# Kernel tuning notes

Hardware: AMD Instinct MI355X
Metric: run time of the kernel (lower is better)

## Reference

```python
import jax, jax.numpy as jnp
import numpy as np

B, T_Q, T_K, H = 16, 1024, 1024, 1024


def _linear_params(key, fan_in, fan_out):
    kw, kb = jax.random.split(key)
    bound = 1.0 / np.sqrt(fan_in)
    W = jax.random.uniform(kw, (fan_out, fan_in), jnp.float32, -bound, bound)
    b = jax.random.uniform(kb, (fan_out,), jnp.float32, -bound, bound)
    return W, b


def setup_inputs() -> dict:
    key = jax.random.key(0)
    ks = jax.random.split(key, 6)
    query = jax.random.normal(ks[0], (B, T_Q, H), jnp.float32)
    keys = jax.random.normal(ks[1], (B, T_K, H), jnp.float32)
    values = jax.random.normal(ks[2], (B, T_K, H), jnp.float32)
    Wq, bq = _linear_params(ks[3], H, H)
    Wk, bk = _linear_params(ks[4], H, H)
    Wo, bo = _linear_params(ks[5], H, H)
    return {"query": query, "keys": keys, "values": values,
            "Wq": Wq, "bq": bq, "Wk": Wk, "bk": bk, "Wo": Wo, "bo": bo}


def reference(query, keys, values, Wq, bq, Wk, bk, Wo, bo):
    # Linear projections (torch Linear: x @ W.T + b)
    q = jnp.einsum('bth,oh->bto', query, Wq) + bq   # (B, T_Q, H)
    k = jnp.einsum('bsh,oh->bso', keys, Wk) + bk    # (B, T_K, H)
    # Unscaled scores -> softmax over key axis (dropout is identity at eval)
    scores = jnp.einsum('bto,bso->bts', q, k)       # (B, T_Q, T_K)
    attn = jax.nn.softmax(scores, axis=-1)
    ctx = jnp.einsum('bts,bsh->bth', attn, values)  # note: raw values, value_fc unused in source
    ctx = ctx / jnp.sqrt(jnp.float32(values.shape[1]))
    out = jnp.einsum('bth,oh->bto', ctx, Wo) + bo
    return out
```

## Files before the change

kernel.cpp:

```cpp
#include <hip/hip_runtime.h>
#include <math.h>

typedef __attribute__((ext_vector_type(4))) float f32x4;
typedef __attribute__((ext_vector_type(8))) _Float16 h16x8;
typedef __attribute__((ext_vector_type(8))) short s16x8;
typedef __attribute__((ext_vector_type(4))) short s16x4;

__device__ inline unsigned short f2h(float f) {
    union { _Float16 h; unsigned short u; } v; v.h = (_Float16)f; return v.u;
}
__device__ inline float h2f(unsigned short u) {
    union { unsigned short u; _Float16 h; } v; v.u = u; return (float)v.h;
}

__device__ inline void async16(const void* g, void* l) {
    __builtin_amdgcn_global_load_lds(
        (const __attribute__((address_space(1))) unsigned int*)g,
        (__attribute__((address_space(3))) unsigned int*)l, 16, 0, 0);
}

__device__ inline void xcd_swizzle(int& bx, int& by, int& bz) {
    const long gx = gridDim.x, gy = gridDim.y;
    const long nwg = gx * gy * (long)gridDim.z;
    const long hw  = ((long)blockIdx.z * gy + blockIdx.y) * gx + blockIdx.x;
    const long qq = nwg >> 3, rr = nwg & 7;
    const long xcd = hw & 7, pos = hw >> 3;
    const long lg = (xcd < rr) ? xcd * (qq + 1) + pos
                               : rr * (qq + 1) + (xcd - rr) * qq + pos;
    bx = (int)(lg % gx);
    const long rem = lg / gx;
    by = (int)(rem % gy);
    bz = (int)(rem / gy);
}

#define BM2 128
#define BN2 256
#define BK2 32

__device__ inline h16x8 ld_frag32(const char* smem, unsigned base, int row, int kbyte) {
    unsigned off = base + (unsigned)(row * 64) + (unsigned)(kbyte ^ ((row & 3) << 4));
    return *(const h16x8*)(smem + off);
}

template<int OM>
__global__ __launch_bounds__(512, 4)
void gemm128(const unsigned short* __restrict__ A,
             const unsigned short* __restrict__ B,
             const float* __restrict__ bias,
             void* __restrict__ C, int N, int lenK, int pitch,
             long sA, long sB, long sC, long sBias, float scale)
{
    __shared__ __align__(16) char smem[49152];

    const int tid  = threadIdx.x;
    const int wv   = tid >> 6;
    const int lane = tid & 63;
    const int wr = wv >> 2, wc = wv & 3;
    const int lrow = lane & 15;
    const int kq16 = (lane >> 4) * 16;

    int bx, by, bz; xcd_swizzle(bx, by, bz);
    const int n0 = bx * BN2;
    const int m0 = by * BM2;

    const unsigned short* Ag = A + (long)bz * sA;
    const unsigned short* Bg = B + (long)bz * sB;
    const int NT = lenK / BK2;

    auto stage = [&](int t) {
        const unsigned db = (unsigned)((t & 1) * 24576);
        {
            int r = tid >> 2, s = tid & 3, ss = s ^ (r & 3);
            async16((const char*)Ag + ((long)(m0 + r) * pitch + t * BK2 + ss * 8) * 2,
                    smem + db + (unsigned)(wv << 10));
        }
#pragma unroll
        for (int l = 0; l < 2; ++l) {
            int idx = l * 512 + tid;
            int r = idx >> 2, s = idx & 3, ss = s ^ (r & 3);
            async16((const char*)Bg + ((long)(n0 + r) * pitch + t * BK2 + ss * 8) * 2,
                    smem + db + 8192u + (unsigned)(l * 8192) + (unsigned)(wv << 10));
        }
    };

    f32x4 acc[4][4];
#pragma unroll
    for (int i = 0; i < 4; ++i)
#pragma unroll
        for (int j = 0; j < 4; ++j) acc[i][j] = (f32x4){0.f, 0.f, 0.f, 0.f};

    const unsigned Abase = (unsigned)(wr * 4096);
    const unsigned Bbase = 8192u + (unsigned)(wc * 4096);

    stage(0);
    __syncthreads();

#pragma unroll 2
    for (int t = 0; t < NT; ++t) {
        const unsigned db = (unsigned)((t & 1) * 24576);
        if (t + 1 < NT) stage(t + 1);
        h16x8 afr[4], bfr[4];
#pragma unroll
        for (int f = 0; f < 4; ++f) {
            afr[f] = ld_frag32(smem, db + Abase, f * 16 + lrow, kq16);
            bfr[f] = ld_frag32(smem, db + Bbase, f * 16 + lrow, kq16);
        }
#pragma unroll
        for (int mi = 0; mi < 4; ++mi)
#pragma unroll
            for (int j = 0; j < 4; ++j)
                acc[mi][j] = __builtin_amdgcn_mfma_f32_16x16x32_f16(
                    afr[mi], bfr[j], acc[mi][j], 0, 0, 0);
        __syncthreads();
    }

#pragma unroll
    for (int j = 0; j < 4; ++j) {
        const int col = n0 + wc * 64 + j * 16 + lrow;
        const float bb = bias ? bias[(long)bz * sBias + col] : 0.f;
#pragma unroll
        for (int mi = 0; mi < 4; ++mi) {
#pragma unroll
            for (int r = 0; r < 4; ++r) {
                const long row = m0 + wr * 64 + mi * 16 + (lane >> 4) * 4 + r;
                const float v = acc[mi][j][r] * scale + bb;
                const long idx = (long)bz * sC + row * (long)N + col;
                if constexpr (OM == 0) ((float*)C)[idx] = v;
                else                   ((unsigned short*)C)[idx] = f2h(v);
            }
        }
    }
}


__global__ __launch_bounds__(256)
void conv2_f16(const float* __restrict__ a, const float* __restrict__ b,
               unsigned short* __restrict__ oa, unsigned short* __restrict__ ob, long n)
{
    const long stride = (long)gridDim.x * 256 * 16;
    const long t0 = ((long)blockIdx.x * 256 + threadIdx.x) * 16;
    for (long i = t0; i < n; i += stride) {
        float4 v0 = *(const float4*)(a + i);
        float4 v1 = *(const float4*)(a + i + 4);
        float4 v2 = *(const float4*)(a + i + 8);
        float4 v3 = *(const float4*)(a + i + 12);
        s16x8 o0 = {(short)f2h(v0.x), (short)f2h(v0.y), (short)f2h(v0.z), (short)f2h(v0.w),
                    (short)f2h(v1.x), (short)f2h(v1.y), (short)f2h(v1.z), (short)f2h(v1.w)};
        s16x8 o1 = {(short)f2h(v2.x), (short)f2h(v2.y), (short)f2h(v2.z), (short)f2h(v2.w),
                    (short)f2h(v3.x), (short)f2h(v3.y), (short)f2h(v3.z), (short)f2h(v3.w)};
        *(s16x8*)(oa + i)     = o0;
        *(s16x8*)(oa + i + 8) = o1;
    }
    for (long i = t0; i < n; i += stride) {
        float4 v0 = *(const float4*)(b + i);
        float4 v1 = *(const float4*)(b + i + 4);
        float4 v2 = *(const float4*)(b + i + 8);
        float4 v3 = *(const float4*)(b + i + 12);
        s16x8 o0 = {(short)f2h(v0.x), (short)f2h(v0.y), (short)f2h(v0.z), (short)f2h(v0.w),
                    (short)f2h(v1.x), (short)f2h(v1.y), (short)f2h(v1.z), (short)f2h(v1.w)};
        s16x8 o1 = {(short)f2h(v2.x), (short)f2h(v2.y), (short)f2h(v2.z), (short)f2h(v2.w),
                    (short)f2h(v3.x), (short)f2h(v3.y), (short)f2h(v3.z), (short)f2h(v3.w)};
        *(s16x8*)(ob + i)     = o0;
        *(s16x8*)(ob + i + 8) = o1;
    }
}

__global__ __launch_bounds__(256)
void conv_f16(const float* __restrict__ in, unsigned short* __restrict__ out, int n)
{
    int i = (blockIdx.x * 256 + threadIdx.x) * 4;
    if (i >= n) return;
    float4 v = *(const float4*)(in + i);
    s16x4 o = {(short)f2h(v.x), (short)f2h(v.y), (short)f2h(v.z), (short)f2h(v.w)};
    *(s16x4*)(out + i) = o;
}

__global__ __launch_bounds__(256)
void transpose_vals(const float* __restrict__ in, unsigned short* __restrict__ out)
{
    __shared__ float tile[32][33];
    const int h0 = blockIdx.x * 32, t0 = blockIdx.y * 32;
    for (int z = blockIdx.z; z < 16; z += gridDim.z) {
        const long base = (long)z * 1024 * 1024;
        __syncthreads();
        for (int i = threadIdx.y; i < 32; i += 8)
            tile[i][threadIdx.x] = in[base + (long)(t0 + i) * 1024 + h0 + threadIdx.x];
        __syncthreads();
        for (int i = threadIdx.y; i < 32; i += 8)
            out[base + (long)(h0 + i) * 1024 + t0 + threadIdx.x] = f2h(tile[threadIdx.x][i]);
    }
}

__global__ __launch_bounds__(256)
void transpose2_f16(const float* __restrict__ inA, const float* __restrict__ inB,
                    unsigned short* __restrict__ outA, unsigned short* __restrict__ outB)
{
    __shared__ float tile[32][33];
    const float* in = blockIdx.z ? inB : inA;
    unsigned short* out = blockIdx.z ? outB : outA;
    const int h0 = blockIdx.x * 32, t0 = blockIdx.y * 32;
    for (int i = threadIdx.y; i < 32; i += 8)
        tile[i][threadIdx.x] = in[(long)(t0 + i) * 1024 + h0 + threadIdx.x];
    __syncthreads();
    for (int i = threadIdx.y; i < 32; i += 8)
        out[(long)(h0 + i) * 1024 + t0 + threadIdx.x] = f2h(tile[threadIdx.x][i]);
}

__global__ __launch_bounds__(256)
void w2_kernel(const float* __restrict__ Wk, const float* __restrict__ bq,
               float* __restrict__ w2)
{
    __shared__ float part[4][64];
    const int tx = threadIdx.x & 63;
    const int ty = threadIdx.x >> 6;
    const int h  = blockIdx.x * 64 + tx;
    float s = 0.f;
    for (int o = ty * 256; o < ty * 256 + 256; ++o)
        s = fmaf(Wk[(long)o * 1024 + h], bq[o], s);
    part[ty][tx] = s;
    __syncthreads();
    if (ty == 0) w2[h] = part[0][tx] + part[1][tx] + part[2][tx] + part[3][tx];
}

__global__ __launch_bounds__(256)
void matvec_v(const unsigned short* __restrict__ Xk, const float* __restrict__ w2,
              float* __restrict__ v)
{
    const int wave = threadIdx.x >> 6, lane = threadIdx.x & 63;
    const long row = (long)blockIdx.x * 4 + wave;
    const unsigned short* p = Xk + row * 1024 + lane * 16;
    float s = 0.f;
#pragma unroll
    for (int c = 0; c < 2; ++c) {
        s16x8 hv = *(const s16x8*)(p + c * 8);
#pragma unroll
        for (int e = 0; e < 8; ++e)
            s = fmaf(h2f((unsigned short)hv[e]), w2[lane * 16 + c * 8 + e], s);
    }
#pragma unroll
    for (int off = 1; off < 64; off <<= 1) s += __shfl_xor(s, off);
    if (lane == 0) v[row] = s;
}

__global__ __launch_bounds__(256)
void reduce4(const float* __restrict__ p, unsigned short* __restrict__ MT)
{
    const long i = ((long)blockIdx.x * 256 + threadIdx.x) * 4;
    const long S = 1024L * 1024;
    float4 a = *(const float4*)(p + i);
    float4 b = *(const float4*)(p + S + i);
    float4 c = *(const float4*)(p + 2 * S + i);
    float4 d = *(const float4*)(p + 3 * S + i);
    s16x4 o = {(short)f2h(a.x + b.x + c.x + d.x), (short)f2h(a.y + b.y + c.y + d.y),
               (short)f2h(a.z + b.z + c.z + d.z), (short)f2h(a.w + b.w + c.w + d.w)};
    *(s16x4*)(MT + i) = o;
}

__global__ __launch_bounds__(256)
void softmax_wave(unsigned short* __restrict__ S)
{
    const int wave = threadIdx.x >> 6, lane = threadIdx.x & 63;
    for (long row = (long)blockIdx.x * 4 + wave; row < 16384; row += (long)gridDim.x * 4) {
        unsigned short* p = S + row * 1024;
        s16x8 ra = *(s16x8*)(p + lane * 8);
        s16x8 rb = *(s16x8*)(p + 512 + lane * 8);
        float va[8], vb[8];
        float m = -3.0e38f;
#pragma unroll
        for (int e = 0; e < 8; ++e) {
            va[e] = h2f((unsigned short)ra[e]); m = fmaxf(m, va[e]);
            vb[e] = h2f((unsigned short)rb[e]); m = fmaxf(m, vb[e]);
        }
#pragma unroll
        for (int off = 1; off < 64; off <<= 1) m = fmaxf(m, __shfl_xor(m, off));
        float s = 0.f;
#pragma unroll
        for (int e = 0; e < 8; ++e) {
            va[e] = expf(va[e] - m); s += va[e];
            vb[e] = expf(vb[e] - m); s += vb[e];
        }
#pragma unroll
        for (int off = 1; off < 64; off <<= 1) s += __shfl_xor(s, off);
        const float inv = 1.f / s;
        s16x8 oa, ob;
#pragma unroll
        for (int e = 0; e < 8; ++e) {
            oa[e] = (short)f2h(va[e] * inv);
            ob[e] = (short)f2h(vb[e] * inv);
        }
        *(s16x8*)(p + lane * 8)       = oa;
        *(s16x8*)(p + 512 + lane * 8) = ob;
    }
}

extern "C" void kernel_launch(void* const* d_in, const int* in_sizes, int n_in,
                              void* d_out, int out_size, void* d_ws, size_t ws_size,
                              hipStream_t stream)
{
    const float* query  = (const float*)d_in[0];
    const float* keys   = (const float*)d_in[1];
    const float* values = (const float*)d_in[2];
    const float* Wq     = (const float*)d_in[3];
    const float* bq     = (const float*)d_in[4];
    const float* Wk     = (const float*)d_in[5];
    const float* bk     = (const float*)d_in[6];
    const float* Wo     = (const float*)d_in[7];
    const float* bo     = (const float*)d_in[8];
    (void)bk;

    const int  T = 1024, H = 1024;
    const long NE = 16384L * 1024;
    const long NW = 1024L * 1024;

    size_t need = (size_t)(NE * 4 + NW * 12 + 40960) * sizeof(unsigned short);
    if (ws_size < need) return;

    unsigned short* ws   = (unsigned short*)d_ws;
    unsigned short* Xq   = ws;
    unsigned short* Xk   = Xq + NE;
    unsigned short* vT   = Xk + NE;
    unsigned short* P1   = vT + NE;
    unsigned short* WqT  = P1 + NE;
    unsigned short* WkT  = WqT + NW;
    unsigned short* Woh  = WkT + NW;
    unsigned short* MT   = Woh + NW;
    float*          part = (float*)(MT + NW);
    float*          w2   = (float*)(MT + NW * 9);
    float*          vvec = w2 + 1024;
    unsigned short* sc   = Xq;
    unsigned short* ctx  = P1;

    conv2_f16<<<2048, 256, 0, stream>>>(query, keys, Xq, Xk, NE);
    transpose2_f16<<<dim3(32, 32, 2), dim3(32, 8), 0, stream>>>(Wq, Wk, WqT, WkT);
    conv_f16<<<1024, 256, 0, stream>>>(Wo, Woh, (int)NW);
    transpose_vals<<<dim3(32, 32, 4), dim3(32, 8), 0, stream>>>(values, vT);
    w2_kernel<<<16, 256, 0, stream>>>(Wk, bq, w2);

    gemm128<0><<<dim3(4, 8, 4), 512, 0, stream>>>(
        WkT, WqT, nullptr, part, 1024, 256, 1024, 256, 256, (long)NW, 0, 1.f);
    reduce4<<<1024, 256, 0, stream>>>(part, MT);

    gemm128<1><<<dim3(4, 128, 1), 512, 0, stream>>>(
        Xq, MT, nullptr, P1, H, H, H, 0, 0, 0, 0, 1.f);

    matvec_v<<<4096, 256, 0, stream>>>(Xk, w2, vvec);

    gemm128<1><<<dim3(4, 8, 16), 512, 0, stream>>>(
        P1, Xk, vvec, sc, T, H, H,
        (long)T * H, (long)T * H, (long)T * T, (long)T, 1.f);

    softmax_wave<<<2048, 256, 0, stream>>>(sc);

    gemm128<1><<<dim3(4, 8, 16), 512, 0, stream>>>(
        sc, vT, nullptr, ctx, H, T, T,
        (long)T * T, (long)T * H, (long)T * H, 0, 1.f / 32.f);

    gemm128<0><<<dim3(4, 128, 1), 512, 0, stream>>>(
        ctx, Woh, bo, d_out, H, H, H, 0, 0, 0, 0, 1.f);
}
```

Baseline: 294.0 us.

## Fuse query fp32-to-fp16 conversion into the first projection GEMM's A-tile load

Adds a GEMM variant that reads the fp32 query directly, converting to fp16 in registers before writing to shared memory, while B is still staged asynchronously. This drops the separate conversion pass over the 16M-element query tensor and its fp16 round trip through global memory. The A path now uses synchronous register loads instead of async LDS loads, so the GEMM reads twice as many bytes for A and may overlap loads less well.

```diff
diff --git a/kernel.cpp b/kernel.cpp
--- a/kernel.cpp
+++ b/kernel.cpp
@@ -132,37 +132,122 @@
     }
 }
 
-
-__global__ __launch_bounds__(256)
-void conv2_f16(const float* __restrict__ a, const float* __restrict__ b,
-               unsigned short* __restrict__ oa, unsigned short* __restrict__ ob, long n)
-{
-    const long stride = (long)gridDim.x * 256 * 16;
-    const long t0 = ((long)blockIdx.x * 256 + threadIdx.x) * 16;
-    for (long i = t0; i < n; i += stride) {
-        float4 v0 = *(const float4*)(a + i);
-        float4 v1 = *(const float4*)(a + i + 4);
-        float4 v2 = *(const float4*)(a + i + 8);
-        float4 v3 = *(const float4*)(a + i + 12);
-        s16x8 o0 = {(short)f2h(v0.x), (short)f2h(v0.y), (short)f2h(v0.z), (short)f2h(v0.w),
-                    (short)f2h(v1.x), (short)f2h(v1.y), (short)f2h(v1.z), (short)f2h(v1.w)};
-        s16x8 o1 = {(short)f2h(v2.x), (short)f2h(v2.y), (short)f2h(v2.z), (short)f2h(v2.w),
-                    (short)f2h(v3.x), (short)f2h(v3.y), (short)f2h(v3.z), (short)f2h(v3.w)};
-        *(s16x8*)(oa + i)     = o0;
-        *(s16x8*)(oa + i + 8) = o1;
-    }
-    for (long i = t0; i < n; i += stride) {
-        float4 v0 = *(const float4*)(b + i);
-        float4 v1 = *(const float4*)(b + i + 4);
-        float4 v2 = *(const float4*)(b + i + 8);
-        float4 v3 = *(const float4*)(b + i + 12);
-        s16x8 o0 = {(short)f2h(v0.x), (short)f2h(v0.y), (short)f2h(v0.z), (short)f2h(v0.w),
-                    (short)f2h(v1.x), (short)f2h(v1.y), (short)f2h(v1.z), (short)f2h(v1.w)};
-        s16x8 o1 = {(short)f2h(v2.x), (short)f2h(v2.y), (short)f2h(v2.z), (short)f2h(v2.w),
-                    (short)f2h(v3.x), (short)f2h(v3.y), (short)f2h(v3.z), (short)f2h(v3.w)};
-        *(s16x8*)(ob + i)     = o0;
-        *(s16x8*)(ob + i + 8) = o1;
-    }
+__global__ __launch_bounds__(512, 4)
+void gemm128_af32(const float* __restrict__ A,
+                  const unsigned short* __restrict__ B,
+                  const float* __restrict__ bias,
+                  unsigned short* __restrict__ C, int N, int lenK, int pitch,
+                  float scale)
+{
+    __shared__ __align__(16) char smem[49152];
+
+    const int tid  = threadIdx.x;
+    const int wv   = tid >> 6;
+    const int lane = tid & 63;
+    const int wr = wv >> 2, wc = wv & 3;
+    const int lrow = lane & 15;
+    const int kq16 = (lane >> 4) * 16;
+
+    int bx, by, bz; xcd_swizzle(bx, by, bz);
+    const int n0 = bx * BN2;
+    const int m0 = by * BM2;
+
+    const int NT = lenK / BK2;
+
+    const int ar = tid >> 2;
+    const int ac = tid & 3;
+    const unsigned aoff = (unsigned)(ar * 64 + ((ac ^ (ar & 3)) << 4));
+
+    auto loadA = [&](int t, float4& x, float4& y) {
+        const float* src = A + (long)(m0 + ar) * pitch + t * BK2 + ac * 8;
+        x = *(const float4*)src;
+        y = *(const float4*)(src + 4);
+    };
+    auto writeA = [&](int t, float4 x, float4 y) {
+        const unsigned db = (unsigned)((t & 1) * 24576);
+        s16x8 o = {(short)f2h(x.x), (short)f2h(x.y), (short)f2h(x.z), (short)f2h(x.w),
+                   (short)f2h(y.x), (short)f2h(y.y), (short)f2h(y.z), (short)f2h(y.w)};
+        *(s16x8*)(smem + db + aoff) = o;
+    };
+    auto stageB = [&](int t) {
+        const unsigned db = (unsigned)((t & 1) * 24576);
+#pragma unroll
+        for (int l = 0; l < 2; ++l) {
+            int idx = l * 512 + tid;
+            int r = idx >> 2, s = idx & 3, ss = s ^ (r & 3);
+            async16((const char*)B + ((long)(n0 + r) * pitch + t * BK2 + ss * 8) * 2,
+                    smem + db + 8192u + (unsigned)(l * 8192) + (unsigned)(wv << 10));
+        }
+    };
+
+    f32x4 acc[4][4];
+#pragma unroll
+    for (int i = 0; i < 4; ++i)
+#pragma unroll
+        for (int j = 0; j < 4; ++j) acc[i][j] = (f32x4){0.f, 0.f, 0.f, 0.f};
+
+    const unsigned Abase = (unsigned)(wr * 4096);
+    const unsigned Bbase = 8192u + (unsigned)(wc * 4096);
+
+    {
+        float4 x, y;
+        loadA(0, x, y);
+        stageB(0);
+        writeA(0, x, y);
+    }
+    __syncthreads();
+
+#pragma unroll 2
+    for (int t = 0; t < NT; ++t) {
+        const unsigned db = (unsigned)((t & 1) * 24576);
+        float4 x, y;
+        if (t + 1 < NT) { loadA(t + 1, x, y); stageB(t + 1); }
+        h16x8 afr[4], bfr[4];
+#pragma unroll
+        for (int f = 0; f < 4; ++f) {
+            afr[f] = ld_frag32(smem, db + Abase, f * 16 + lrow, kq16);
+            bfr[f] = ld_frag32(smem, db + Bbase, f * 16 + lrow, kq16);
+        }
+#pragma unroll
+        for (int mi = 0; mi < 4; ++mi)
+#pragma unroll
+            for (int j = 0; j < 4; ++j)
+                acc[mi][j] = __builtin_amdgcn_mfma_f32_16x16x32_f16(
+                    afr[mi], bfr[j], acc[mi][j], 0, 0, 0);
+        if (t + 1 < NT) writeA(t + 1, x, y);
+        __syncthreads();
+    }
+
+#pragma unroll
+    for (int j = 0; j < 4; ++j) {
+        const int col = n0 + wc * 64 + j * 16 + lrow;
+        const float bb = bias ? bias[col] : 0.f;
+#pragma unroll
+        for (int mi = 0; mi < 4; ++mi) {
+#pragma unroll
+            for (int r = 0; r < 4; ++r) {
+                const long row = m0 + wr * 64 + mi * 16 + (lane >> 4) * 4 + r;
+                C[row * (long)N + col] = f2h(acc[mi][j][r] * scale + bb);
+            }
+        }
+    }
+}
+
+
+__global__ __launch_bounds__(256)
+void conv1_f16(const float* __restrict__ in, unsigned short* __restrict__ out)
+{
+    const long i = ((long)blockIdx.x * 256 + threadIdx.x) * 16;
+    float4 v0 = *(const float4*)(in + i);
+    float4 v1 = *(const float4*)(in + i + 4);
+    float4 v2 = *(const float4*)(in + i + 8);
+    float4 v3 = *(const float4*)(in + i + 12);
+    s16x8 o0 = {(short)f2h(v0.x), (short)f2h(v0.y), (short)f2h(v0.z), (short)f2h(v0.w),
+                (short)f2h(v1.x), (short)f2h(v1.y), (short)f2h(v1.z), (short)f2h(v1.w)};
+    s16x8 o1 = {(short)f2h(v2.x), (short)f2h(v2.y), (short)f2h(v2.z), (short)f2h(v2.w),
+                (short)f2h(v3.x), (short)f2h(v3.y), (short)f2h(v3.z), (short)f2h(v3.w)};
+    *(s16x8*)(out + i)     = o0;
+    *(s16x8*)(out + i + 8) = o1;
 }
 
 __global__ __launch_bounds__(256)
@@ -316,8 +401,8 @@
     if (ws_size < need) return;
 
     unsigned short* ws   = (unsigned short*)d_ws;
-    unsigned short* Xq   = ws;
-    unsigned short* Xk   = Xq + NE;
+    unsigned short* sc   = ws;
+    unsigned short* Xk   = sc + NE;
     unsigned short* vT   = Xk + NE;
     unsigned short* P1   = vT + NE;
     unsigned short* WqT  = P1 + NE;
@@ -327,10 +412,9 @@
     float*          part = (float*)(MT + NW);
     float*          w2   = (float*)(MT + NW * 9);
     float*          vvec = w2 + 1024;
-    unsigned short* sc   = Xq;
     unsigned short* ctx  = P1;
 
-    conv2_f16<<<2048, 256, 0, stream>>>(query, keys, Xq, Xk, NE);
+    conv1_f16<<<4096, 256, 0, stream>>>(keys, Xk);
     transpose2_f16<<<dim3(32, 32, 2), dim3(32, 8), 0, stream>>>(Wq, Wk, WqT, WkT);
     conv_f16<<<1024, 256, 0, stream>>>(Wo, Woh, (int)NW);
     transpose_vals<<<dim3(32, 32, 4), dim3(32, 8), 0, stream>>>(values, vT);
@@ -340,8 +424,8 @@
         WkT, WqT, nullptr, part, 1024, 256, 1024, 256, 256, (long)NW, 0, 1.f);
     reduce4<<<1024, 256, 0, stream>>>(part, MT);
 
-    gemm128<1><<<dim3(4, 128, 1), 512, 0, stream>>>(
-        Xq, MT, nullptr, P1, H, H, H, 0, 0, 0, 0, 1.f);
+    gemm128_af32<<<dim3(4, 128, 1), 512, 0, stream>>>(
+        query, MT, nullptr, P1, H, H, H, 1.f);
 
     matvec_v<<<4096, 256, 0, stream>>>(Xk, w2, vvec);
 
```

Measured after the change: 304.8 us. 3.6% more time.
